# Kernel tuning notes

Hardware: AMD Instinct MI355X
Metric: run time of the kernel (lower is better)

## Reference

```python
import jax, jax.numpy as jnp
import numpy as np

N = 100000   # nodes
E = 1600000  # edges (avg degree 16)
IN = 128     # in_channels
H = 64       # num_hidden -> conv1 out = 2*H = 128
RRELU_SLOPE = (1.0 / 8.0 + 1.0 / 3.0) / 2.0  # F.rrelu eval: mean of (lower, upper)


def setup_inputs() -> dict:
    key = jax.random.key(0)
    k1, k2, k3, k4 = jax.random.split(key, 4)
    x = jax.random.normal(k1, (N, IN), dtype=jnp.float32)
    edge_index = jax.random.randint(k2, (2, E), 0, N, dtype=jnp.int32)
    # Glorot-ish init for the two GCN linear layers (PyG GCNConv has weight + bias)
    W1 = jax.random.normal(k3, (IN, 2 * H), dtype=jnp.float32) * (1.0 / np.sqrt(IN))
    b1 = jnp.zeros((2 * H,), dtype=jnp.float32)
    W2 = jax.random.normal(k4, (2 * H, H), dtype=jnp.float32) * (1.0 / np.sqrt(2 * H))
    b2 = jnp.zeros((H,), dtype=jnp.float32)
    return {"x": x, "edge_index": edge_index, "W1": W1, "b1": b1, "W2": W2, "b2": b2}


def _gcn_conv(x, row, col, norm, W, b, n):
    # PyG GCNConv: transform, gather source nodes, scale by sym norm, scatter-add to targets
    h = x @ W                                   # [N, out]
    msg = h[row] * norm[:, None]                # [E+N, out] gathered messages
    return jax.ops.segment_sum(msg, col, num_segments=n) + b


def reference(x, edge_index, W1, b1, W2, b2):
    n = x.shape[0]
    loops = jnp.arange(n, dtype=edge_index.dtype)
    row = jnp.concatenate([edge_index[0], loops])  # sources (with self-loops)
    col = jnp.concatenate([edge_index[1], loops])  # targets (with self-loops)
    deg = jax.ops.segment_sum(jnp.ones_like(col, dtype=x.dtype), col, num_segments=n)
    dinv = jnp.where(deg > 0, jax.lax.rsqrt(deg), 0.0)
    norm = dinv[row] * dinv[col]                  # deg^{-1/2}[u] * deg^{-1/2}[v]
    h = _gcn_conv(x, row, col, norm, W1, b1, n)
    h = jnp.where(h >= 0, h, RRELU_SLOPE * h)     # rrelu (eval mode)
    return _gcn_conv(h, row, col, norm, W2, b2, n)
```

## Files before the change

### kernel.cpp

```cpp
#include <hip/hip_runtime.h>


#define C_IN   128
#define C_MID  128
#define C_OUT2 64
#define SLOT_CAP 64
#define SORT_SH  9
#define SORT_W   196
#define SORT_CAP 16384
#define P1_EPT   8

typedef __attribute__((ext_vector_type(8))) short short8;
typedef __attribute__((ext_vector_type(4))) float floatx4;
typedef __attribute__((ext_vector_type(2))) float f32x2;

__device__ __constant__ float kSlope = 0.22916666666666666f;

__device__ __forceinline__ unsigned short f2bf(float f) {
    unsigned u = __builtin_bit_cast(unsigned, f);
    u = (u + 0x7fffu + ((u >> 16) & 1u)) >> 16;
    return (unsigned short)u;
}
__device__ __forceinline__ f32x2 bfpair(int x) {
    return (f32x2){__builtin_bit_cast(float, (unsigned)x << 16),
                   __builtin_bit_cast(float, (unsigned)(x & 0xffff0000))};
}

__global__ __launch_bounds__(256) void sort_gemm1_kernel(
        const int* __restrict__ ei, int2* __restrict__ sorted,
        int* __restrict__ bcur,
        const float* __restrict__ X,
        const float* __restrict__ W1, const float* __restrict__ W2,
        ushort* __restrict__ W2T, ushort* __restrict__ h1,
        int E, int n, int p1b, int g1b) {
    __shared__ __align__(16) ushort Ws[64 * 136];
    const int tid = threadIdx.x;

    if (blockIdx.x < p1b) {
        int* hist = (int*)Ws;
        int* goff = hist + SORT_W;
        int* cur  = goff + SORT_W;
        for (int i = tid; i < SORT_W; i += 256) { hist[i] = 0; cur[i] = 0; }
        __syncthreads();
        const int base = blockIdx.x * (P1_EPT * 256);
#pragma unroll
        for (int k = 0; k < P1_EPT; ++k) {
            int e = base + k * 256 + tid;
            if (e < E) atomicAdd(&hist[ei[E + e] >> SORT_SH], 1);
        }
        __syncthreads();
        for (int i = tid; i < SORT_W; i += 256)
            if (hist[i]) goff[i] = atomicAdd(&bcur[i], hist[i]);
        __syncthreads();
#pragma unroll
        for (int k = 0; k < P1_EPT; ++k) {
            int e = base + k * 256 + tid;
            if (e < E) {
                int v = ei[E + e], u = ei[e];
                int b = v >> SORT_SH;
                int p = goff[b] + atomicAdd(&cur[b], 1);
                if (p < SORT_CAP) sorted[(size_t)b * SORT_CAP + p] = (int2){u, v};
            }
        }
        return;
    }
    if (blockIdx.x >= p1b + g1b) {
        int t = (blockIdx.x - p1b - g1b) * 256 + tid;
        if (t < C_OUT2 * C_MID) {
            int nn = t >> 7, k = t & 127;
            W2T[t] = f2bf(W2[k * C_OUT2 + nn]);
        }
        return;
    }
    const int wave = tid >> 6, lane = tid & 63;
    const int m = lane & 15, q = lane >> 4;
    const int row0 = (blockIdx.x - p1b) * 64;
    const int rowA = min(row0 + wave * 16 + m, n - 1);

    short8 af[4];
#pragma unroll
    for (int s = 0; s < 4; ++s) {
        const float* xp = X + (size_t)rowA * C_IN + s * 32 + q * 8;
        float4 a0 = *(const float4*)xp;
        float4 a1 = *(const float4*)(xp + 4);
        union { unsigned short us[8]; short8 v; } t;
        t.us[0] = f2bf(a0.x); t.us[1] = f2bf(a0.y); t.us[2] = f2bf(a0.z); t.us[3] = f2bf(a0.w);
        t.us[4] = f2bf(a1.x); t.us[5] = f2bf(a1.y); t.us[6] = f2bf(a1.z); t.us[7] = f2bf(a1.w);
        af[s] = t.v;
    }
    floatx4 acc[8];
#pragma unroll
    for (int c = 0; c < 8; ++c) acc[c] = (floatx4){0.f, 0.f, 0.f, 0.f};

#pragma unroll
    for (int h = 0; h < 2; ++h) {
        __syncthreads();
        for (int i = 0; i < 32; ++i) {
            int idx = i * 256 + tid;
            int k = idx >> 6, rl = idx & 63;
            Ws[rl * 136 + k] = f2bf(W1[k * C_MID + h * 64 + rl]);
        }
        __syncthreads();
#pragma unroll
        for (int s = 0; s < 4; ++s)
#pragma unroll
            for (int c = 0; c < 4; ++c) {
                short8 bf = *(short8*)&Ws[(c * 16 + m) * 136 + s * 32 + q * 8];
                acc[h * 4 + c] = __builtin_amdgcn_mfma_f32_16x16x32_bf16(af[s], bf, acc[h * 4 + c], 0, 0, 0);
            }
    }
#pragma unroll
    for (int c = 0; c < 8; ++c)
#pragma unroll
        for (int i = 0; i < 4; ++i) {
            int rr = row0 + wave * 16 + q * 4 + i;
            if (rr < n) h1[(size_t)rr * C_MID + c * 16 + m] = f2bf(acc[c][i]);
        }
}

__global__ __launch_bounds__(256) void csr_kernel(
        const int2* __restrict__ sorted, const int* __restrict__ bcur,
        int* __restrict__ cnt, float* __restrict__ dinv,
        int* __restrict__ slots, int n) {
    __shared__ int lc[512];
    const int b = blockIdx.x, tid = threadIdx.x;
    const int base_v = b << SORT_SH;
    for (int i = tid; i < 512; i += 256) lc[i] = 0;
    __syncthreads();
    const int nb = min(bcur[b], SORT_CAP);
    const int2* src = sorted + (size_t)b * SORT_CAP;
    for (int i = tid; i < nb; i += 256) {
        int2 e = src[i];
        int pos = atomicAdd(&lc[e.y - base_v], 1);
        if (pos < SLOT_CAP - 1) slots[(size_t)e.y * SLOT_CAP + pos] = e.x;
    }
    __syncthreads();
    for (int i = tid; i < 512; i += 256) {
        int v = base_v + i;
        if (v < n) {
            int deg = lc[i];
            int st = min(deg, SLOT_CAP - 1);
            slots[(size_t)v * SLOT_CAP + st] = v;
            cnt[v] = st + 1;
            dinv[v] = rsqrtf((float)(deg + 1));
        }
    }
}

template <int C, bool DO_RRELU, int OUT_MODE>
__global__ __launch_bounds__(256) void agg_kernel(const ushort* __restrict__ H,
                                                  const int* __restrict__ slots,
                                                  const int* __restrict__ cnt,
                                                  const float* __restrict__ dinv,
                                                  const float* __restrict__ bias,
                                                  void* __restrict__ outv, int n,
                                                  const ushort* __restrict__ W2T) {
    constexpr int GS = C / 8;
    constexpr int NG = 64 / GS;
    constexpr int NCH = 24 / NG;
    __shared__ ushort Hs[OUT_MODE == 2 ? 8 * 136 : 8];
    __shared__ int    Vs[8];
    const int wave = threadIdx.x >> 6, lane = threadIdx.x & 63;
    int vA = blockIdx.x * 8 + wave * 2;
    if constexpr (OUT_MODE == 2) {
        vA = min(vA, n - 2);
    } else {
        if (vA >= n) return;
    }
    const int vB = (vA + 1 < n) ? vA + 1 : vA;

    int rawA = slots[(size_t)vA * SLOT_CAP + lane];
    int rawB = slots[(size_t)vB * SLOT_CAP + lane];
    const int limA = cnt[vA], limB = cnt[vB];
    const float dvA = dinv[vA], dvB = dinv[vB];
    const int uA = min(max(rawA, 0), n - 1);
    const int uB = min(max(rawB, 0), n - 1);
    const float wA_l = dinv[uA] * dvA;
    const float wB_l = dinv[uB] * dvB;
    const int lastA = limA - 1, lastB = limB - 1;

    const int g = lane / GS, s = lane % GS;

    float wwA[NCH], wwB[NCH];
    int4 ddA[NCH], ddB[NCH];
#pragma unroll
    for (int t = 0; t < NCH; ++t) {
        int jj = t * NG + g;
        int cA = jj < lastA ? jj : lastA;
        int cB = jj < lastB ? jj : lastB;
        int usA = __shfl(uA, cA), usB = __shfl(uB, cB);
        float wsA = __shfl(wA_l, cA), wsB = __shfl(wB_l, cB);
        wwA[t] = (jj < limA) ? wsA : 0.f;
        wwB[t] = (jj < limB) ? wsB : 0.f;
        ddA[t] = *(const int4*)(H + (size_t)usA * C + s * 8);
        ddB[t] = *(const int4*)(H + (size_t)usB * C + s * 8);
    }
    __builtin_amdgcn_sched_barrier(0);

    f32x2 accA[4], accB[4];
#pragma unroll
    for (int k = 0; k < 4; ++k) { accA[k] = (f32x2){0.f, 0.f}; accB[k] = (f32x2){0.f, 0.f}; }
#pragma unroll
    for (int t = 0; t < NCH; ++t) {
        accA[0] += bfpair(ddA[t].x) * wwA[t]; accA[1] += bfpair(ddA[t].y) * wwA[t];
        accA[2] += bfpair(ddA[t].z) * wwA[t]; accA[3] += bfpair(ddA[t].w) * wwA[t];
        accB[0] += bfpair(ddB[t].x) * wwB[t]; accB[1] += bfpair(ddB[t].y) * wwB[t];
        accB[2] += bfpair(ddB[t].z) * wwB[t]; accB[3] += bfpair(ddB[t].w) * wwB[t];
    }
    for (int j = 24; j < limA; j += NG) {
        int jj = j + g;
        int c = jj < lastA ? jj : lastA;
        int u = __shfl(uA, c);
        float wv = __shfl(wA_l, c);
        float wgt = (jj < limA) ? wv : 0.f;
        const int4 d = *(const int4*)(H + (size_t)u * C + s * 8);
        accA[0] += bfpair(d.x) * wgt; accA[1] += bfpair(d.y) * wgt;
        accA[2] += bfpair(d.z) * wgt; accA[3] += bfpair(d.w) * wgt;
    }
    for (int j = 24; j < limB; j += NG) {
        int jj = j + g;
        int c = jj < lastB ? jj : lastB;
        int u = __shfl(uB, c);
        float wv = __shfl(wB_l, c);
        float wgt = (jj < limB) ? wv : 0.f;
        const int4 d = *(const int4*)(H + (size_t)u * C + s * 8);
        accB[0] += bfpair(d.x) * wgt; accB[1] += bfpair(d.y) * wgt;
        accB[2] += bfpair(d.z) * wgt; accB[3] += bfpair(d.w) * wgt;
    }

    float a[8], b8[8];
#pragma unroll
    for (int k = 0; k < 4; ++k) {
        a[2 * k] = accA[k].x; a[2 * k + 1] = accA[k].y;
        b8[2 * k] = accB[k].x; b8[2 * k + 1] = accB[k].y;
    }
#pragma unroll
    for (int k = 0; k < 8; ++k)
#pragma unroll
        for (int off = GS; off < 64; off <<= 1) {
            a[k] += __shfl_xor(a[k], off);
            b8[k] += __shfl_xor(b8[k], off);
        }

    if constexpr (OUT_MODE == 2) {
        if (g < 2) {
            const int v = (g == 0) ? vA : vB;
            union { ushort us[8]; int4 v4; } o;
#pragma unroll
            for (int k = 0; k < 8; ++k) {
                float t = (g == 0) ? a[k] : b8[k];
                t += bias[s * 8 + k];
                if (DO_RRELU) t = (t >= 0.f) ? t : t * kSlope;
                o.us[k] = f2bf(t);
            }
            *(int4*)&Hs[(wave * 2 + g) * 136 + s * 8] = o.v4;
            if (s == 0) Vs[wave * 2 + g] = v;
        }
        __syncthreads();
        const int m2 = lane & 15, q2 = lane >> 4;
        floatx4 acc2 = (floatx4){0.f, 0.f, 0.f, 0.f};
#pragma unroll
        for (int s2 = 0; s2 < 4; ++s2) {
            short8 af = *(short8*)&Hs[m2 * 136 + s2 * 32 + q2 * 8];
            short8 bf = *(const short8*)(W2T + (size_t)(wave * 16 + m2) * C_MID + s2 * 32 + q2 * 8);
            acc2 = __builtin_amdgcn_mfma_f32_16x16x32_bf16(af, bf, acc2, 0, 0, 0);
        }
        ushort* Y2 = (ushort*)outv;
#pragma unroll
        for (int i = 0; i < 4; ++i) {
            int node = q2 * 4 + i;
            if (node < 8)
                Y2[(size_t)Vs[node] * C_OUT2 + wave * 16 + m2] = f2bf(acc2[i]);
        }
    } else if (g < 2) {
        const int v = (g == 0) ? vA : vB;
        float r[8];
#pragma unroll
        for (int k = 0; k < 8; ++k) {
            float t = (g == 0) ? a[k] : b8[k];
            r[k] = t + bias[s * 8 + k];
            if (DO_RRELU) r[k] = (r[k] >= 0.f) ? r[k] : r[k] * kSlope;
        }
        float* op = (float*)outv + (size_t)v * C + s * 8;
        *(float4*)op       = (float4){r[0], r[1], r[2], r[3]};
        *(float4*)(op + 4) = (float4){r[4], r[5], r[6], r[7]};
    }
}

extern "C" void kernel_launch(void* const* d_in, const int* in_sizes, int n_in,
                              void* d_out, int out_size, void* d_ws, size_t ws_size,
                              hipStream_t stream) {
    const float* x  = (const float*)d_in[0];
    const int*   ei = (const int*)d_in[1];
    const float* W1 = (const float*)d_in[2];
    const float* b1 = (const float*)d_in[3];
    const float* W2 = (const float*)d_in[4];
    const float* b2 = (const float*)d_in[5];
    const int n = in_sizes[0] / C_IN;
    const int E = in_sizes[1] / 2;

    char* w = (char*)d_ws;
    auto alloc = [&](size_t bytes) -> char* {
        char* p = w; w += (bytes + 255) & ~(size_t)255; return p;
    };
    int*    cnt    = (int*)alloc((size_t)n * 4);
    float*  dinv   = (float*)alloc((size_t)n * 4);
    int*    slots  = (int*)alloc((size_t)n * SLOT_CAP * 4);
    ushort* h1     = (ushort*)alloc((size_t)n * C_MID * 2);
    ushort* h3     = (ushort*)alloc((size_t)n * C_OUT2 * 2);
    ushort* W2T    = (ushort*)alloc((size_t)C_OUT2 * C_MID * 2);
    int2*   sorted = (int2*)alloc((size_t)SORT_W * SORT_CAP * 8);
    int*    bcur   = (int*)alloc((size_t)SORT_W * 4);

    const int p1b = (E + P1_EPT * 256 - 1) / (P1_EPT * 256);
    const int g1b = (n + 63) / 64;
    const int prep2_blocks = (C_OUT2 * C_MID + 255) / 256;

    hipMemsetAsync(bcur, 0, (size_t)SORT_W * 4, stream);
    sort_gemm1_kernel<<<p1b + g1b + prep2_blocks, 256, 0, stream>>>(
        ei, sorted, bcur, x, W1, W2, W2T, h1, E, n, p1b, g1b);
    csr_kernel<<<SORT_W, 256, 0, stream>>>(sorted, bcur, cnt, dinv, slots, n);
    agg_kernel<C_MID, true, 2><<<(n + 7) / 8, 256, 0, stream>>>(
        h1, slots, cnt, dinv, b1, h3, n, W2T);
    agg_kernel<C_OUT2, false, 0><<<(n + 7) / 8, 256, 0, stream>>>(
        h3, slots, cnt, dinv, b2, d_out, n, nullptr);
}
```

Before: 270.3 us.

## Replace bucket sort plus CSR pass with direct global-atomic slot build

Removes the two-phase bucket sort, which staged edges into per-bucket arrays and then a separate CSR kernel binned them into per-node slots using shared-memory atomics. Each edge now does a global atomicAdd on its target's counter and writes its source straight into the slot list, and a lightweight per-node kernel appends the self-loop and computes dinv. This drops the intermediate sorted buffer and one full read/write pass over the edges. In exchange it relies on heavily contended global atomics with random scattered slot writes, and the order of neighbours within each slot list becomes nondeterministic.

```diff
diff --git a/kernel.cpp b/kernel.cpp
--- a/kernel.cpp
+++ b/kernel.cpp
@@ -5,10 +5,7 @@
 #define C_MID  128
 #define C_OUT2 64
 #define SLOT_CAP 64
-#define SORT_SH  9
-#define SORT_W   196
-#define SORT_CAP 16384
-#define P1_EPT   8
+#define P1_EPT   4
 
 typedef __attribute__((ext_vector_type(8))) short short8;
 typedef __attribute__((ext_vector_type(4))) float floatx4;
@@ -26,46 +23,31 @@
                    __builtin_bit_cast(float, (unsigned)(x & 0xffff0000))};
 }
 
-__global__ __launch_bounds__(256) void sort_gemm1_kernel(
-        const int* __restrict__ ei, int2* __restrict__ sorted,
-        int* __restrict__ bcur,
+__global__ __launch_bounds__(256) void build_gemm1_kernel(
+        const int* __restrict__ ei, int* __restrict__ cnt,
+        int* __restrict__ slots,
         const float* __restrict__ X,
         const float* __restrict__ W1, const float* __restrict__ W2,
         ushort* __restrict__ W2T, ushort* __restrict__ h1,
-        int E, int n, int p1b, int g1b) {
+        int E, int n, int bb, int g1b) {
     __shared__ __align__(16) ushort Ws[64 * 136];
     const int tid = threadIdx.x;
 
-    if (blockIdx.x < p1b) {
-        int* hist = (int*)Ws;
-        int* goff = hist + SORT_W;
-        int* cur  = goff + SORT_W;
-        for (int i = tid; i < SORT_W; i += 256) { hist[i] = 0; cur[i] = 0; }
-        __syncthreads();
+    if (blockIdx.x < bb) {
         const int base = blockIdx.x * (P1_EPT * 256);
-#pragma unroll
-        for (int k = 0; k < P1_EPT; ++k) {
-            int e = base + k * 256 + tid;
-            if (e < E) atomicAdd(&hist[ei[E + e] >> SORT_SH], 1);
-        }
-        __syncthreads();
-        for (int i = tid; i < SORT_W; i += 256)
-            if (hist[i]) goff[i] = atomicAdd(&bcur[i], hist[i]);
-        __syncthreads();
 #pragma unroll
         for (int k = 0; k < P1_EPT; ++k) {
             int e = base + k * 256 + tid;
             if (e < E) {
                 int v = ei[E + e], u = ei[e];
-                int b = v >> SORT_SH;
-                int p = goff[b] + atomicAdd(&cur[b], 1);
-                if (p < SORT_CAP) sorted[(size_t)b * SORT_CAP + p] = (int2){u, v};
+                int pos = atomicAdd(&cnt[v], 1);
+                if (pos < SLOT_CAP - 1) slots[(size_t)v * SLOT_CAP + pos] = u;
             }
         }
         return;
     }
-    if (blockIdx.x >= p1b + g1b) {
-        int t = (blockIdx.x - p1b - g1b) * 256 + tid;
+    if (blockIdx.x >= bb + g1b) {
+        int t = (blockIdx.x - bb - g1b) * 256 + tid;
         if (t < C_OUT2 * C_MID) {
             int nn = t >> 7, k = t & 127;
             W2T[t] = f2bf(W2[k * C_OUT2 + nn]);
@@ -74,7 +56,7 @@
     }
     const int wave = tid >> 6, lane = tid & 63;
     const int m = lane & 15, q = lane >> 4;
-    const int row0 = (blockIdx.x - p1b) * 64;
+    const int row0 = (blockIdx.x - bb) * 64;
     const int rowA = min(row0 + wave * 16 + m, n - 1);
 
     short8 af[4];
@@ -118,32 +100,16 @@
         }
 }
 
-__global__ __launch_bounds__(256) void csr_kernel(
-        const int2* __restrict__ sorted, const int* __restrict__ bcur,
+__global__ __launch_bounds__(256) void finish_kernel(
         int* __restrict__ cnt, float* __restrict__ dinv,
         int* __restrict__ slots, int n) {
-    __shared__ int lc[512];
-    const int b = blockIdx.x, tid = threadIdx.x;
-    const int base_v = b << SORT_SH;
-    for (int i = tid; i < 512; i += 256) lc[i] = 0;
-    __syncthreads();
-    const int nb = min(bcur[b], SORT_CAP);
-    const int2* src = sorted + (size_t)b * SORT_CAP;
-    for (int i = tid; i < nb; i += 256) {
-        int2 e = src[i];
-        int pos = atomicAdd(&lc[e.y - base_v], 1);
-        if (pos < SLOT_CAP - 1) slots[(size_t)e.y * SLOT_CAP + pos] = e.x;
-    }
-    __syncthreads();
-    for (int i = tid; i < 512; i += 256) {
-        int v = base_v + i;
-        if (v < n) {
-            int deg = lc[i];
-            int st = min(deg, SLOT_CAP - 1);
-            slots[(size_t)v * SLOT_CAP + st] = v;
-            cnt[v] = st + 1;
-            dinv[v] = rsqrtf((float)(deg + 1));
-        }
+    int v = blockIdx.x * 256 + threadIdx.x;
+    if (v < n) {
+        int deg = cnt[v];
+        int st = min(deg, SLOT_CAP - 1);
+        slots[(size_t)v * SLOT_CAP + st] = v;
+        cnt[v] = st + 1;
+        dinv[v] = rsqrtf((float)(deg + 1));
     }
 }
 
@@ -309,17 +275,15 @@
     ushort* h1     = (ushort*)alloc((size_t)n * C_MID * 2);
     ushort* h3     = (ushort*)alloc((size_t)n * C_OUT2 * 2);
     ushort* W2T    = (ushort*)alloc((size_t)C_OUT2 * C_MID * 2);
-    int2*   sorted = (int2*)alloc((size_t)SORT_W * SORT_CAP * 8);
-    int*    bcur   = (int*)alloc((size_t)SORT_W * 4);
-
-    const int p1b = (E + P1_EPT * 256 - 1) / (P1_EPT * 256);
+
+    const int bb  = (E + P1_EPT * 256 - 1) / (P1_EPT * 256);
     const int g1b = (n + 63) / 64;
     const int prep2_blocks = (C_OUT2 * C_MID + 255) / 256;
 
-    hipMemsetAsync(bcur, 0, (size_t)SORT_W * 4, stream);
-    sort_gemm1_kernel<<<p1b + g1b + prep2_blocks, 256, 0, stream>>>(
-        ei, sorted, bcur, x, W1, W2, W2T, h1, E, n, p1b, g1b);
-    csr_kernel<<<SORT_W, 256, 0, stream>>>(sorted, bcur, cnt, dinv, slots, n);
+    hipMemsetAsync(cnt, 0, (size_t)n * 4, stream);
+    build_gemm1_kernel<<<bb + g1b + prep2_blocks, 256, 0, stream>>>(
+        ei, cnt, slots, x, W1, W2, W2T, h1, E, n, bb, g1b);
+    finish_kernel<<<(n + 255) / 256, 256, 0, stream>>>(cnt, dinv, slots, n);
     agg_kernel<C_MID, true, 2><<<(n + 7) / 8, 256, 0, stream>>>(
         h1, slots, cnt, dinv, b1, h3, n, W2T);
     agg_kernel<C_OUT2, false, 0><<<(n + 7) / 8, 256, 0, stream>>>(
```

Measured after the change: 370.6 us. +37.1%, slower.
